# Kernel tuning notes

Measured on AMD Instinct MI355X. Metric: run time of the kernel, lower is better.

Reference implementation:

```python
import jax, jax.numpy as jnp
import numpy as np

B, E, H, C, R = 16, 1024, 1024, 64, 64  # batch, input_size, hidden_size, context_size, context_rank
H4 = 4 * H


def setup_inputs() -> dict:
    key = jax.random.key(0)
    ks = jax.random.split(key, 12)
    n = lambda k, shape, scale: jax.random.normal(k, shape, dtype=jnp.float32) * scale
    return {
        'x': n(ks[0], (B, E), 1.0),
        'h': n(ks[1], (B, H), 1.0),
        'c': n(ks[2], (B, H), 1.0),
        'context': n(ks[3], (B, C), 1.0),
        'Wi': n(ks[4], (E, H4), 0.02),
        'Wi_b': n(ks[5], (H4,), 0.02),
        'Wh': n(ks[6], (H, H4), 0.02),
        'Wh_b': n(ks[7], (H4,), 0.02),
        'AZ_il': n(ks[8], (C, E, R), 0.02),
        'AZ_ir': n(ks[9], (R, H4, C), 0.02),
        'AZ_hl': n(ks[10], (C, H, R), 0.02),
        'AZ_hr': n(ks[11], (R, H4, C), 0.02),
    }


def reference(x, h, c, context, Wi, Wi_b, Wh, Wh_b, AZ_il, AZ_ir, AZ_hl, AZ_hr):
    hs = Wh.shape[0]
    # compute_context_weights: per-sample low-rank weight perturbations
    lhs_i = jnp.einsum('bc,cer->ber', context, AZ_il)      # [B,E,R]
    rhs_i = jnp.einsum('bc,rjc->brj', context, AZ_ir)      # [B,R,4H]
    A_i = jnp.einsum('ber,brj->bej', lhs_i, rhs_i)         # [B,E,4H]
    lhs_h = jnp.einsum('bc,chr->bhr', context, AZ_hl)      # [B,H,R]
    rhs_h = jnp.einsum('bc,rjc->brj', context, AZ_hr)      # [B,R,4H]
    A_h = jnp.einsum('bhr,brj->bhj', lhs_h, rhs_h)         # [B,H,4H]
    # forward (faithful to original: context weights are multiplied by 0)
    Wi_eff = 0.0 * A_i + Wi                                # [B,E,4H]
    Wh_eff = 0.0 * A_h + Wh                                # [B,H,4H]
    ifgo = (jnp.einsum('be,bej->bj', x, Wi_eff) + Wi_b
            + jnp.einsum('bh,bhj->bj', h, Wh_eff) + Wh_b)  # [B,4H]
    i = jax.nn.sigmoid(ifgo[:, :hs])
    f = jax.nn.sigmoid(ifgo[:, hs:2 * hs])
    g = jnp.tanh(ifgo[:, 2 * hs:3 * hs])
    o = jax.nn.sigmoid(ifgo[:, 3 * hs:])
    c_new = f * c + i * g
    h_new = o * jnp.tanh(c_new)
    return (h_new, c_new)
```

## Files before the change

### kernel.cpp

```cpp
#include <hip/hip_runtime.h>
#include <stdint.h>

#define H4_ 4096
#define B_  16

__global__ __launch_bounds__(256) void k_fused2(
    const float* __restrict__ x, const float* __restrict__ h,
    const float* __restrict__ cin,
    const float* __restrict__ Wi, const float* __restrict__ Wh,
    const float* __restrict__ Wi_b, const float* __restrict__ Wh_b,
    float* __restrict__ out)
{
    __shared__ float a_lds[256][16];
    __shared__ float red[16][16][16];
    __shared__ float gsum[16][16];

    const int bl = blockIdx.x;
    const int j0 = (bl & 7) * 128 + (bl >> 3) * 4;
    const int t  = threadIdx.x;
    const int g  = t & 3;
    const int bq = (t >> 2) & 3;
    const int ks = t >> 4;

    float acc[4][4];
    #pragma unroll
    for (int r = 0; r < 4; r++)
        #pragma unroll
        for (int c = 0; c < 4; c++) acc[r][c] = 0.f;

    for (int m = 0; m < 8; ++m) {
        const float* A  = (m < 4) ? x : h;
        const float* W  = (m < 4) ? Wi : Wh;
        const int    e0 = (m & 3) * 256;

        {
            const int b = t & 15, kc = t >> 4;
            const float* src = A + b * 1024 + e0 + kc * 16;
            float4 v0 = *(const float4*)(src);
            float4 v1 = *(const float4*)(src + 4);
            float4 v2 = *(const float4*)(src + 8);
            float4 v3 = *(const float4*)(src + 12);
            const float vv[16] = { v0.x, v0.y, v0.z, v0.w, v1.x, v1.y, v1.z, v1.w,
                                   v2.x, v2.y, v2.z, v2.w, v3.x, v3.y, v3.z, v3.w };
            #pragma unroll
            for (int j = 0; j < 16; j++) a_lds[kc * 16 + j][b] = vv[j];
        }
        __syncthreads();

        const float* wp = W + (size_t)e0 * H4_ + g * 1024 + j0;
        #pragma unroll
        for (int i = 0; i < 16; i++) {
            const int kl = ks * 16 + i;
            float4 w = *(const float4*)(wp + (size_t)kl * H4_);
            float4 a = *(const float4*)&a_lds[kl][bq * 4];
            acc[0][0] += a.x * w.x; acc[0][1] += a.x * w.y; acc[0][2] += a.x * w.z; acc[0][3] += a.x * w.w;
            acc[1][0] += a.y * w.x; acc[1][1] += a.y * w.y; acc[1][2] += a.y * w.z; acc[1][3] += a.y * w.w;
            acc[2][0] += a.z * w.x; acc[2][1] += a.z * w.y; acc[2][2] += a.z * w.z; acc[2][3] += a.z * w.w;
            acc[3][0] += a.w * w.x; acc[3][1] += a.w * w.y; acc[3][2] += a.w * w.z; acc[3][3] += a.w * w.w;
        }
        __syncthreads();
    }

    #pragma unroll
    for (int r = 0; r < 4; r++)
        *(float4*)&red[ks][bq * 4 + r][g * 4] =
            make_float4(acc[r][0], acc[r][1], acc[r][2], acc[r][3]);
    __syncthreads();
    {
        const int b = t >> 4, c16 = t & 15;
        float s = 0.f;
        #pragma unroll
        for (int kk = 0; kk < 16; kk++) s += red[kk][b][c16];
        gsum[b][c16] = s;
    }
    __syncthreads();

    if (t < 64) {
        const int b = t >> 2, jj = t & 3;
        const int j = j0 + jj;
        const float s0 = gsum[b][jj]      + Wi_b[j]        + Wh_b[j];
        const float s1 = gsum[b][4 + jj]  + Wi_b[1024 + j] + Wh_b[1024 + j];
        const float s2 = gsum[b][8 + jj]  + Wi_b[2048 + j] + Wh_b[2048 + j];
        const float s3 = gsum[b][12 + jj] + Wi_b[3072 + j] + Wh_b[3072 + j];
        const float ig = 1.f / (1.f + __expf(-s0));
        const float fg = 1.f / (1.f + __expf(-s1));
        const float gg = tanhf(s2);
        const float og = 1.f / (1.f + __expf(-s3));
        const float cv = cin[b * 1024 + j];
        const float cn = fg * cv + ig * gg;
        const float hn = og * tanhf(cn);
        out[b * 1024 + j]         = hn;
        out[16384 + b * 1024 + j] = cn;
    }
}

extern "C" void kernel_launch(void* const* d_in, const int* in_sizes, int n_in,
                              void* d_out, int out_size, void* d_ws, size_t ws_size,
                              hipStream_t stream) {
    (void)in_sizes; (void)n_in; (void)out_size; (void)d_ws; (void)ws_size;
    const float* x    = (const float*)d_in[0];
    const float* h    = (const float*)d_in[1];
    const float* c    = (const float*)d_in[2];
    const float* Wi   = (const float*)d_in[4];
    const float* Wi_b = (const float*)d_in[5];
    const float* Wh   = (const float*)d_in[6];
    const float* Wh_b = (const float*)d_in[7];

    k_fused2<<<256, 256, 0, stream>>>(x, h, c, Wi, Wh, Wi_b, Wh_b,
                                      (float*)d_out);
}
```

Measured before the change: 202.3 us.

## Split-K GEMM into workspace partials followed by a separate reduce-and-activate kernel

Replaces the single fused kernel with a two-kernel split-K scheme. The first kernel uses 512 blocks, each covering a 32-row K slice, and writes 64 partial [16x4096] sums to the workspace. The second kernel reduces those partials, adds the biases and applies the LSTM gates. The aim is more parallelism for streaming the 32MB of weights. In exchange it writes and re-reads about 16MB of partials and adds a second launch. The old fused kernel is kept as a fallback when the workspace is too small, with its inner unroll reduced to 4.

```diff
diff --git a/kernel.cpp b/kernel.cpp
--- a/kernel.cpp
+++ b/kernel.cpp
@@ -3,6 +3,96 @@
 
 #define H4_ 4096
 #define B_  16
+#define SPLITS_ 64
+
+__global__ __launch_bounds__(256) void k1_gemm(
+    const float* __restrict__ x, const float* __restrict__ h,
+    const float* __restrict__ Wi, const float* __restrict__ Wh,
+    float* __restrict__ part)
+{
+    __shared__ float a_lds[32][16];
+
+    const int bl = blockIdx.x;
+    const int q  = bl & 7;
+    const int s  = bl >> 3;
+    const int t  = threadIdx.x;
+
+    const float* A = (s < 32) ? x : h;
+    const float* W = (s < 32) ? Wi : Wh;
+    const int e0 = (s & 31) * 32;
+
+    {
+        const int b = t & 15, r0 = t >> 4;
+        a_lds[r0][b]      = A[b * 1024 + e0 + r0];
+        a_lds[r0 + 16][b] = A[b * 1024 + e0 + r0 + 16];
+    }
+    __syncthreads();
+
+    const int j = q * 512 + t * 2;
+    const float* wp = W + (size_t)e0 * H4_ + j;
+
+    float2 acc[16];
+    #pragma unroll
+    for (int b = 0; b < 16; b++) acc[b] = make_float2(0.f, 0.f);
+
+    #pragma unroll 16
+    for (int kl = 0; kl < 32; kl++) {
+        const float2 w  = *(const float2*)(wp + (size_t)kl * H4_);
+        const float4 a0 = *(const float4*)&a_lds[kl][0];
+        const float4 a1 = *(const float4*)&a_lds[kl][4];
+        const float4 a2 = *(const float4*)&a_lds[kl][8];
+        const float4 a3 = *(const float4*)&a_lds[kl][12];
+        const float av[16] = { a0.x,a0.y,a0.z,a0.w, a1.x,a1.y,a1.z,a1.w,
+                               a2.x,a2.y,a2.z,a2.w, a3.x,a3.y,a3.z,a3.w };
+        #pragma unroll
+        for (int b = 0; b < 16; b++) {
+            acc[b].x += av[b] * w.x;
+            acc[b].y += av[b] * w.y;
+        }
+    }
+
+    float* dst = part + (size_t)s * B_ * H4_ + j;
+    #pragma unroll
+    for (int b = 0; b < 16; b++)
+        *(float2*)(dst + (size_t)b * H4_) = acc[b];
+}
+
+__global__ __launch_bounds__(256) void k2_act(
+    const float* __restrict__ part, const float* __restrict__ c,
+    const float* __restrict__ Wi_b, const float* __restrict__ Wh_b,
+    float* __restrict__ out)
+{
+    __shared__ float gl[4][64];
+
+    const int blk = blockIdx.x;
+    const int b   = blk >> 4;
+    const int j0  = (blk & 15) * 64;
+    const int t   = threadIdx.x;
+    const int g   = t >> 6, jj = t & 63;
+    const int col = g * 1024 + j0 + jj;
+
+    float acc = Wi_b[col] + Wh_b[col];
+    const float* pp = part + (size_t)b * H4_ + col;
+    #pragma unroll 16
+    for (int ss = 0; ss < SPLITS_; ss++)
+        acc += pp[(size_t)ss * B_ * H4_];
+    gl[g][jj] = acc;
+    __syncthreads();
+
+    if (t < 64) {
+        const int j = j0 + t;
+        const float s0 = gl[0][t], s1 = gl[1][t], s2 = gl[2][t], s3 = gl[3][t];
+        const float ig = 1.f / (1.f + __expf(-s0));
+        const float fg = 1.f / (1.f + __expf(-s1));
+        const float gg = tanhf(s2);
+        const float og = 1.f / (1.f + __expf(-s3));
+        const float cv = c[b * 1024 + j];
+        const float cn = fg * cv + ig * gg;
+        const float hn = og * tanhf(cn);
+        out[b * 1024 + j]         = hn;
+        out[16384 + b * 1024 + j] = cn;
+    }
+}
 
 __global__ __launch_bounds__(256) void k_fused2(
     const float* __restrict__ x, const float* __restrict__ h,
@@ -32,7 +122,6 @@
         const float* A  = (m < 4) ? x : h;
         const float* W  = (m < 4) ? Wi : Wh;
         const int    e0 = (m & 3) * 256;
-
         {
             const int b = t & 15, kc = t >> 4;
             const float* src = A + b * 1024 + e0 + kc * 16;
@@ -43,12 +132,11 @@
             const float vv[16] = { v0.x, v0.y, v0.z, v0.w, v1.x, v1.y, v1.z, v1.w,
                                    v2.x, v2.y, v2.z, v2.w, v3.x, v3.y, v3.z, v3.w };
             #pragma unroll
-            for (int j = 0; j < 16; j++) a_lds[kc * 16 + j][b] = vv[j];
+            for (int jj = 0; jj < 16; jj++) a_lds[kc * 16 + jj][b] = vv[jj];
         }
         __syncthreads();
-
         const float* wp = W + (size_t)e0 * H4_ + g * 1024 + j0;
-        #pragma unroll
+        #pragma unroll 4
         for (int i = 0; i < 16; i++) {
             const int kl = ks * 16 + i;
             float4 w = *(const float4*)(wp + (size_t)kl * H4_);
@@ -68,10 +156,10 @@
     __syncthreads();
     {
         const int b = t >> 4, c16 = t & 15;
-        float s = 0.f;
+        float sum = 0.f;
         #pragma unroll
-        for (int kk = 0; kk < 16; kk++) s += red[kk][b][c16];
-        gsum[b][c16] = s;
+        for (int kk = 0; kk < 16; kk++) sum += red[kk][b][c16];
+        gsum[b][c16] = sum;
     }
     __syncthreads();
 
@@ -97,7 +185,7 @@
 extern "C" void kernel_launch(void* const* d_in, const int* in_sizes, int n_in,
                               void* d_out, int out_size, void* d_ws, size_t ws_size,
                               hipStream_t stream) {
-    (void)in_sizes; (void)n_in; (void)out_size; (void)d_ws; (void)ws_size;
+    (void)in_sizes; (void)n_in; (void)out_size;
     const float* x    = (const float*)d_in[0];
     const float* h    = (const float*)d_in[1];
     const float* c    = (const float*)d_in[2];
@@ -106,6 +194,14 @@
     const float* Wh   = (const float*)d_in[6];
     const float* Wh_b = (const float*)d_in[7];
 
-    k_fused2<<<256, 256, 0, stream>>>(x, h, c, Wi, Wh, Wi_b, Wh_b,
-                                      (float*)d_out);
-}
+    float* part = (float*)d_ws;
+    float* out  = (float*)d_out;
+
+    const size_t need = (size_t)SPLITS_ * B_ * H4_ * sizeof(float);
+    if (ws_size >= need) {
+        k1_gemm<<<512, 256, 0, stream>>>(x, h, Wi, Wh, part);
+        k2_act<<<256, 256, 0, stream>>>(part, c, Wi_b, Wh_b, out);
+    } else {
+        k_fused2<<<64 * 4, 256, 0, stream>>>(x, h, c, Wi, Wh, Wi_b, Wh_b, out);
+    }
+}
```

Result: faster. 184.8 us (-8.7%).
